# Kernel tuning notes

Hardware: AMD Instinct MI355X
Metric: run time of the kernel (lower is better)

The kernel has to match this reference:

```python
import jax, jax.numpy as jnp
import numpy as np

N_NODES = 100000
N_EDGES = 1600000
IN_FEATS = 256
N_HIDDEN = 128
N_CLASSES = 40


def setup_inputs() -> dict:
    key = jax.random.key(0)
    k1, k2, k3, k4, k5 = jax.random.split(key, 5)
    features = jax.random.normal(k1, (N_NODES, IN_FEATS), dtype=jnp.float32)
    edge_src = jax.random.randint(k2, (N_EDGES,), 0, N_NODES, dtype=jnp.int64)
    edge_dst = jax.random.randint(k3, (N_EDGES,), 0, N_NODES, dtype=jnp.int64)
    # GraphConv weights (Glorot-ish scaling)
    W1 = jax.random.normal(k4, (IN_FEATS, N_HIDDEN), dtype=jnp.float32) / np.sqrt(IN_FEATS)
    b1 = jnp.zeros((N_HIDDEN,), dtype=jnp.float32)
    W2 = jax.random.normal(k5, (N_HIDDEN, N_CLASSES), dtype=jnp.float32) / np.sqrt(N_HIDDEN)
    b2 = jnpspace = None
    b2 = jnp.zeros((N_CLASSES,), dtype=jnp.float32)
    return {"features": features, "edge_src": edge_src, "edge_dst": edge_dst,
            "W1": W1, "b1": b1, "W2": W2, "b2": b2}


def _degree_norms(edge_src, edge_dst, n_nodes):
    ones = jnp.ones(edge_src.shape[0], dtype=jnp.float32)
    deg_out = jax.ops.segment_sum(ones, edge_src, num_segments=n_nodes)
    deg_in = jax.ops.segment_sum(ones, edge_dst, num_segments=n_nodes)
    norm_src = jax.lax.rsqrt(jnp.clip(deg_out, 1.0))  # D_out^{-1/2}
    norm_dst = jax.lax.rsqrt(jnp.clip(deg_in, 1.0))   # D_in^{-1/2}
    return norm_src, norm_dst


def _graph_conv(x, W, b, edge_src, edge_dst, norm_src, norm_dst, activation=None):
    # DGL GraphConv norm='both': out = D_in^{-1/2} A D_out^{-1/2} (x W) + b
    h = (x @ W) * norm_src[:, None]                       # transform then src-normalize
    agg = jax.ops.segment_sum(h[edge_src], edge_dst,
                              num_segments=x.shape[0])    # sparse neighbor aggregation
    out = agg * norm_dst[:, None] + b
    if activation is not None:
        out = activation(out)
    return out


def reference(features, edge_src, edge_dst, W1, b1, W2, b2):
    norm_src, norm_dst = _degree_norms(edge_src, edge_dst, features.shape[0])
    h = _graph_conv(features, W1, b1, edge_src, edge_dst, norm_src, norm_dst,
                    activation=jax.nn.relu)
    # dropout is identity in eval-mode reference
    out = _graph_conv(h, W2, b2, edge_src, edge_dst, norm_src, norm_dst)
    return out
```

## Files before the change

kernel.cpp:

```cpp
#include <hip/hip_runtime.h>
#include <hip/hip_bf16.h>
#include <hip/hip_fp16.h>

#define NN 100000
#define NE 1600000
#define KF 256
#define NH 128
#define NC 40
#define CMAX 63

#define NBLK_P 512
#define PCHUNK (NE / NBLK_P)
#define BUK 256
#define NBUK ((NN + BUK - 1) / BUK)
#define CAP 6144

typedef __attribute__((ext_vector_type(8))) short bf16x8;
typedef __attribute__((ext_vector_type(4))) float f32x4;


__device__ __forceinline__ float ldf(const void* p, size_t i, bool bf){
  return bf ? __bfloat162float(((const __hip_bfloat16*)p)[i]) : ((const float*)p)[i];
}
__device__ __forceinline__ void splitbf(float f, short* h, short* lo){
  union { float f; unsigned int u; } a; a.f = f;
  *h = (short)(a.u >> 16);
  union { unsigned int u; float f; } c; c.u = a.u & 0xffff0000u;
  union { float f; unsigned int u; } d; d.f = f - c.f;
  *lo = (short)(d.u >> 16);
}

__global__ void k_sniff_edges(const unsigned int* __restrict__ e, unsigned int* __restrict__ flags){
  __shared__ unsigned int sh[256];
  unsigned int v = 0;
  for (int i = blockIdx.x * 256 + threadIdx.x; i < NE / 2; i += gridDim.x * 256)
    v |= e[2 * i + 1];
  sh[threadIdx.x] = v;
  __syncthreads();
  for (int off = 128; off; off >>= 1){
    if (threadIdx.x < off) sh[threadIdx.x] |= sh[threadIdx.x + off];
    __syncthreads();
  }
  if (threadIdx.x == 0 && sh[0]) atomicOr(&flags[0], sh[0]);
}

__global__ void k_sniff_float(const unsigned int* __restrict__ w, unsigned int* __restrict__ flags){
  __shared__ unsigned int sh[256];
  unsigned int hits = 0;
  for (int i = blockIdx.x * 256 + threadIdx.x; i < (1 << 20); i += gridDim.x * 256){
    unsigned int b = (w[i] >> 7) & 0xFFu;
    hits += (b >= 118u && b <= 130u) ? 1u : 0u;
  }
  sh[threadIdx.x] = hits;
  __syncthreads();
  for (int off = 128; off; off >>= 1){
    if (threadIdx.x < off) sh[threadIdx.x] += sh[threadIdx.x + off];
    __syncthreads();
  }
  if (threadIdx.x == 0) atomicAdd(&flags[1], sh[0]);
}

__device__ __forceinline__ int edge_at(const void* p, int e, bool is64){
  return is64 ? (int)((const long long*)p)[e] : ((const int*)p)[e];
}
__device__ __forceinline__ bool f_isbf(const unsigned int* flags){ return flags[1] > (1u << 19); }

__global__ __launch_bounds__(256) void k_part(const void* __restrict__ src,
    const void* __restrict__ dst, const unsigned int* __restrict__ flags,
    int* __restrict__ deg_out, int* __restrict__ gcur, unsigned int* __restrict__ part){
  __shared__ int cnt[NBUK];
  __shared__ int base[NBUK];
  const bool is64 = (flags[0] == 0u);
  const int beg = blockIdx.x * PCHUNK;
  const int end = min(beg + PCHUNK, NE);
  for (int t = threadIdx.x; t < NBUK; t += 256) cnt[t] = 0;
  __syncthreads();
  for (int e = beg + threadIdx.x; e < end; e += 256){
    int d = edge_at(dst, e, is64);
    atomicAdd(&cnt[d >> 8], 1);
  }
  __syncthreads();
  for (int t = threadIdx.x; t < NBUK; t += 256){
    int c = cnt[t];
    base[t] = c ? atomicAdd(&gcur[t], c) : 0;
    cnt[t] = 0;
  }
  __syncthreads();
  for (int e = beg + threadIdx.x; e < end; e += 256){
    int d = edge_at(dst, e, is64);
    int s = edge_at(src, e, is64);
    atomicAdd(&deg_out[s], 1);
    int b = d >> 8;
    int pos = base[b] + atomicAdd(&cnt[b], 1);
    if (pos < CAP)
      part[(size_t)b * CAP + pos] = ((unsigned int)s << 8) | (unsigned int)(d & 255);
  }
}

__global__ __launch_bounds__(256) void k_csr(const unsigned int* __restrict__ part,
    const int* __restrict__ gcur, int* __restrict__ fill, int* __restrict__ csr_t){
  __shared__ int rows[256 * CMAX];
  __shared__ int fl[256];
  const int b = blockIdx.x;
  fl[threadIdx.x] = 0;
  __syncthreads();
  const int n = min(gcur[b], CAP);
  for (int i = threadIdx.x; i < n; i += 256){
    unsigned int e = part[(size_t)b * CAP + i];
    int r = (int)(e & 255u);
    int s = (int)(e >> 8);
    int pos = atomicAdd(&fl[r], 1);
    if (pos < CMAX) rows[r * CMAX + pos] = s;
  }
  __syncthreads();
  const int node0 = b * BUK;
  const int node  = node0 + threadIdx.x;
  if (node < NN) fill[node] = fl[threadIdx.x];
  __syncthreads();
  for (int off = 128; off; off >>= 1){
    if (threadIdx.x < off) fl[threadIdx.x] = max(fl[threadIdx.x], fl[threadIdx.x + off]);
    __syncthreads();
  }
  const int mx = min(fl[0], CMAX);
  for (int c = 0; c < mx; c++)
    if (node < NN) csr_t[(size_t)c * NN + node] = rows[threadIdx.x * CMAX + c];
}

__global__ void k_norms(const int* __restrict__ deg_out, const int* __restrict__ fill,
                        float* __restrict__ nsrc, float* __restrict__ ndst){
  int i = blockIdx.x * 256 + threadIdx.x;
  if (i < NN){
    nsrc[i] = rsqrtf(fmaxf((float)deg_out[i], 1.f));
    ndst[i] = rsqrtf(fmaxf((float)fill[i], 1.f));
  }
}

__global__ void k_w1s_f32(const void* __restrict__ W1, const unsigned int* __restrict__ flags,
                          bf16x8* __restrict__ w1h, bf16x8* __restrict__ w1l){
  if (f_isbf(flags)) return;
  int idx = blockIdx.x * 256 + threadIdx.x;
  if (idx >= 4096) return;
  int l    = idx & 63;
  int tile = idx >> 6;
  int kt   = tile >> 3;
  int nt   = tile & 7;
  int krow = kt * 32 + (l >> 4) * 8;
  int col  = nt * 16 + (l & 15);
  const float* w = (const float*)W1;
  bf16x8 vh, vl;
  #pragma unroll
  for (int j = 0; j < 8; j++){
    short h, lo;
    splitbf(w[(size_t)(krow + j) * NH + col], &h, &lo);
    vh[j] = h; vl[j] = lo;
  }
  w1h[idx] = vh;
  w1l[idx] = vl;
}

__global__ __launch_bounds__(256) void k_gemm1_mf32(const float* __restrict__ feat,
    const bf16x8* __restrict__ w1h, const bf16x8* __restrict__ w1l,
    const unsigned int* __restrict__ flags,
    const float* __restrict__ nsrc, __half* __restrict__ h1){
  const int t  = threadIdx.x;
  const int wv = t >> 6;
  const int l  = t & 63;
  const int row0 = blockIdx.x * 128 + wv * 32;
  const int ar0 = row0 + (l & 15);
  const int ar1 = ar0 + 16;
  const float* fp0 = feat + (size_t)min(ar0, NN - 1) * KF + (l >> 4) * 8;
  const float* fp1 = feat + (size_t)min(ar1, NN - 1) * KF + (l >> 4) * 8;

  f32x4 acc[2][8];
  #pragma unroll
  for (int g = 0; g < 2; g++)
    #pragma unroll
    for (int n = 0; n < 8; n++) acc[g][n] = (f32x4){0.f, 0.f, 0.f, 0.f};

  for (int kt = 0; kt < 8; kt++){
    float4 u0 = *(const float4*)(fp0 + kt * 32);
    float4 u1 = *(const float4*)(fp0 + kt * 32 + 4);
    float4 v0 = *(const float4*)(fp1 + kt * 32);
    float4 v1 = *(const float4*)(fp1 + kt * 32 + 4);
    bf16x8 a0h, a0l, a1h, a1l;
    {
      const float* uf = (const float*)&u0;
      const float* vf = (const float*)&v0;
      #pragma unroll
      for (int j = 0; j < 4; j++){
        short h, lo;
        splitbf(uf[j], &h, &lo); a0h[j] = h; a0l[j] = lo;
        splitbf(vf[j], &h, &lo); a1h[j] = h; a1l[j] = lo;
      }
      const float* uf2 = (const float*)&u1;
      const float* vf2 = (const float*)&v1;
      #pragma unroll
      for (int j = 0; j < 4; j++){
        short h, lo;
        splitbf(uf2[j], &h, &lo); a0h[4 + j] = h; a0l[4 + j] = lo;
        splitbf(vf2[j], &h, &lo); a1h[4 + j] = h; a1l[4 + j] = lo;
      }
    }
    #pragma unroll
    for (int n = 0; n < 8; n++){
      bf16x8 bh = w1h[(kt * 8 + n) * 64 + l];
      bf16x8 bl = w1l[(kt * 8 + n) * 64 + l];
      acc[0][n] = __builtin_amdgcn_mfma_f32_16x16x32_bf16(a0h, bh, acc[0][n], 0, 0, 0);
      acc[0][n] = __builtin_amdgcn_mfma_f32_16x16x32_bf16(a0l, bh, acc[0][n], 0, 0, 0);
      acc[0][n] = __builtin_amdgcn_mfma_f32_16x16x32_bf16(a0h, bl, acc[0][n], 0, 0, 0);
      acc[1][n] = __builtin_amdgcn_mfma_f32_16x16x32_bf16(a1h, bh, acc[1][n], 0, 0, 0);
      acc[1][n] = __builtin_amdgcn_mfma_f32_16x16x32_bf16(a1l, bh, acc[1][n], 0, 0, 0);
      acc[1][n] = __builtin_amdgcn_mfma_f32_16x16x32_bf16(a1h, bl, acc[1][n], 0, 0, 0);
    }
  }
  const int col = l & 15;
  #pragma unroll
  for (int g = 0; g < 2; g++){
    const int rbase = row0 + g * 16 + (l >> 4) * 4;
    #pragma unroll
    for (int i = 0; i < 4; i++){
      int r = rbase + i;
      if (r < NN){
        float s = nsrc[r];
        #pragma unroll
        for (int n = 0; n < 8; n++)
          h1[(size_t)r * NH + n * 16 + col] = __float2half_rn(acc[g][n][i] * s);
      }
    }
  }
}

__global__ __launch_bounds__(256) void k_agg1v(const int* __restrict__ csr_t,
    const int* __restrict__ fill, const float* __restrict__ ndst,
    const __half* __restrict__ h1, const void* __restrict__ b1,
    const unsigned int* __restrict__ flags, float* __restrict__ x1){
  const bool isbf = f_isbf(flags);
  const int node = blockIdx.x * 4 + (threadIdx.x >> 6);
  if (node >= NN) return;
  const int l  = threadIdx.x & 63;
  const int g  = l >> 4;
  const int sl = l & 15;
  const int deg = min(fill[node], CMAX);
  float a[8] = {0.f,0.f,0.f,0.f,0.f,0.f,0.f,0.f};
  int c0 = 0;
  for (; c0 + 8 <= deg; c0 += 8){
    int s0 = csr_t[(size_t)(c0 + g) * NN + node];
    int s1 = csr_t[(size_t)(c0 + 4 + g) * NN + node];
    uint4 u0 = *(const uint4*)(h1 + (size_t)s0 * NH + sl * 8);
    uint4 u1 = *(const uint4*)(h1 + (size_t)s1 * NH + sl * 8);
    const __half2* h0 = (const __half2*)&u0;
    const __half2* hp1 = (const __half2*)&u1;
    #pragma unroll
    for (int j = 0; j < 4; j++){
      float2 v0 = __half22float2(h0[j]);
      float2 v1 = __half22float2(hp1[j]);
      a[2*j]   += v0.x + v1.x;
      a[2*j+1] += v0.y + v1.y;
    }
  }
  for (; c0 < deg; c0 += 4){
    int c = c0 + g;
    if (c < deg){
      int s = csr_t[(size_t)c * NN + node];
      uint4 u = *(const uint4*)(h1 + (size_t)s * NH + sl * 8);
      const __half2* hp = (const __half2*)&u;
      #pragma unroll
      for (int j = 0; j < 4; j++){
        float2 v = __half22float2(hp[j]);
        a[2*j]   += v.x;
        a[2*j+1] += v.y;
      }
    }
  }
  #pragma unroll
  for (int j = 0; j < 8; j++){
    a[j] += __shfl_xor(a[j], 16);
    a[j] += __shfl_xor(a[j], 32);
  }
  if (g == 0){
    float nd = ndst[node];
    float o[8];
    #pragma unroll
    for (int j = 0; j < 8; j++)
      o[j] = fmaxf(a[j] * nd + ldf(b1, sl * 8 + j, isbf), 0.f);
    float4* xp = (float4*)(x1 + (size_t)node * NH + sl * 8);
    xp[0] = make_float4(o[0], o[1], o[2], o[3]);
    xp[1] = make_float4(o[4], o[5], o[6], o[7]);
  }
}

__global__ __launch_bounds__(256) void k_gemm2(const float* __restrict__ x1,
    const void* __restrict__ W2, const unsigned int* __restrict__ flags,
    const float* __restrict__ nsrc, __half* __restrict__ h2){
  const bool isbf = f_isbf(flags);
  __shared__ float Xs[128][68];
  __shared__ float Ws[64][44];
  const int t = threadIdx.x;
  const int row0 = blockIdx.x * 128;
  const int cg = t & 7;
  const int rg = t >> 3;
  float acc[4][5];
  #pragma unroll
  for (int i = 0; i < 4; i++)
    #pragma unroll
    for (int j = 0; j < 5; j++) acc[i][j] = 0.f;

  for (int kc = 0; kc < NH; kc += 64){
    #pragma unroll
    for (int q0 = 0; q0 < 8; q0++){
      int q  = t + q0 * 256;
      int r  = q >> 4;
      int kq = (q & 15) * 4;
      int grow = row0 + r;
      float4 v;
      if (grow < NN) v = *(const float4*)(x1 + (size_t)grow * NH + kc + kq);
      else { v.x = v.y = v.z = v.w = 0.f; }
      *(float4*)&Xs[r][kq] = v;
    }
    #pragma unroll
    for (int q0 = 0; q0 < 10; q0++){
      int idx = t + q0 * 256;
      int k = idx / 40;
      int c = idx - k * 40;
      Ws[k][c] = ldf(W2, (size_t)(kc + k) * NC + c, isbf);
    }
    __syncthreads();
    #pragma unroll 4
    for (int k = 0; k < 64; k++){
      float a0 = Xs[rg*4+0][k];
      float a1 = Xs[rg*4+1][k];
      float a2 = Xs[rg*4+2][k];
      float a3 = Xs[rg*4+3][k];
      float b[5];
      #pragma unroll
      for (int j = 0; j < 5; j++) b[j] = Ws[k][cg*5 + j];
      #pragma unroll
      for (int j = 0; j < 5; j++){
        acc[0][j] += a0 * b[j];
        acc[1][j] += a1 * b[j];
        acc[2][j] += a2 * b[j];
        acc[3][j] += a3 * b[j];
      }
    }
    __syncthreads();
  }
  #pragma unroll
  for (int i = 0; i < 4; i++){
    int r = row0 + rg*4 + i;
    if (r < NN){
      float s = nsrc[r];
      #pragma unroll
      for (int j = 0; j < 5; j++)
        h2[(size_t)r * NC + cg*5 + j] = __float2half_rn(acc[i][j] * s);
    }
  }
}

__global__ __launch_bounds__(256) void k_agg2v(const int* __restrict__ csr_t,
    const int* __restrict__ fill, const float* __restrict__ ndst,
    const __half* __restrict__ h2, const void* __restrict__ b2,
    const unsigned int* __restrict__ flags, float* __restrict__ out){
  const bool isbf = f_isbf(flags);
  const int node = blockIdx.x * 4 + (threadIdx.x >> 6);
  if (node >= NN) return;
  const int l  = threadIdx.x & 63;
  const int g  = l >> 4;
  const int sl = l & 15;
  const int deg = min(fill[node], CMAX);
  float a[4] = {0.f,0.f,0.f,0.f};
  if (sl < 10){
    int c0 = 0;
    for (; c0 + 8 <= deg; c0 += 8){
      int s0 = csr_t[(size_t)(c0 + g) * NN + node];
      int s1 = csr_t[(size_t)(c0 + 4 + g) * NN + node];
      uint2 u0 = *(const uint2*)(h2 + (size_t)s0 * NC + sl * 4);
      uint2 u1 = *(const uint2*)(h2 + (size_t)s1 * NC + sl * 4);
      const __half2* h0 = (const __half2*)&u0;
      const __half2* hp1 = (const __half2*)&u1;
      #pragma unroll
      for (int j = 0; j < 2; j++){
        float2 v0 = __half22float2(h0[j]);
        float2 v1 = __half22float2(hp1[j]);
        a[2*j]   += v0.x + v1.x;
        a[2*j+1] += v0.y + v1.y;
      }
    }
    for (; c0 < deg; c0 += 4){
      int c = c0 + g;
      if (c < deg){
        int s = csr_t[(size_t)c * NN + node];
        uint2 u = *(const uint2*)(h2 + (size_t)s * NC + sl * 4);
        const __half2* hp = (const __half2*)&u;
        #pragma unroll
        for (int j = 0; j < 2; j++){
          float2 v = __half22float2(hp[j]);
          a[2*j]   += v.x;
          a[2*j+1] += v.y;
        }
      }
    }
  }
  #pragma unroll
  for (int j = 0; j < 4; j++){
    a[j] += __shfl_xor(a[j], 16);
    a[j] += __shfl_xor(a[j], 32);
  }
  if (g == 0 && sl < 10){
    float nd = ndst[node];
    float4 o;
    o.x = a[0] * nd + ldf(b2, sl * 4 + 0, isbf);
    o.y = a[1] * nd + ldf(b2, sl * 4 + 1, isbf);
    o.z = a[2] * nd + ldf(b2, sl * 4 + 2, isbf);
    o.w = a[3] * nd + ldf(b2, sl * 4 + 3, isbf);
    *(float4*)(out + (size_t)node * NC + sl * 4) = o;
  }
}

extern "C" void kernel_launch(void* const* d_in, const int* in_sizes, int n_in,
                              void* d_out, int out_size, void* d_ws, size_t ws_size,
                              hipStream_t stream) {
  const long long SZ_FEAT = (long long)NN * KF, SZ_E = NE, SZ_W1 = (long long)KF * NH,
                  SZ_B1 = NH, SZ_W2 = (long long)NH * NC, SZ_B2 = NC;
  int i_feat = -1, i_e1 = -1, i_e2 = -1, i_W1 = -1, i_b1 = -1, i_W2 = -1, i_b2 = -1;
  auto m = [](long long s, long long z){ return s == z || s == 4*z || s == 8*z || s == 2*z; };
  for (int i = 0; i < n_in; i++){
    long long s = in_sizes[i];
    if      (m(s, SZ_FEAT)) i_feat = i;
    else if (m(s, SZ_E))    { if (i_e1 < 0) i_e1 = i; else i_e2 = i; }
    else if (m(s, SZ_W1))   i_W1 = i;
    else if (m(s, SZ_B1))   i_b1 = i;
    else if (m(s, SZ_W2))   i_W2 = i;
    else if (m(s, SZ_B2))   i_b2 = i;
  }
  if (i_feat < 0 || i_e2 < 0 || i_W1 < 0 || i_b1 < 0 || i_W2 < 0 || i_b2 < 0){
    i_feat = 0; i_e1 = 1; i_e2 = 2; i_W1 = 3; i_b1 = 4; i_W2 = 5; i_b2 = 6;
  }
  const void* feat = d_in[i_feat];
  const void* esrc = d_in[i_e1];
  const void* edst = d_in[i_e2];
  const void* W1   = d_in[i_W1];
  const void* b1   = d_in[i_b1];
  const void* W2   = d_in[i_W2];
  const void* b2   = d_in[i_b2];
  float* out = (float*)d_out;

  int* deg_out        = (int*)d_ws;
  int* fill           = deg_out + NN;
  unsigned int* flags = (unsigned int*)(fill + NN);
  int* gcur           = (int*)(flags + 4);
  float* norm_src     = (float*)(gcur + 400);
  float* norm_dst     = norm_src + NN;
  int* csr_t          = (int*)(norm_dst + NN);
  __half* h1          = (__half*)(csr_t + (size_t)CMAX * NN);
  float* x1           = (float*)(h1 + (size_t)NN * NH);
  __half* h2          = h1;
  unsigned int* part  = (unsigned int*)x1;
  bf16x8* w1h         = (bf16x8*)((char*)x1 + (16u << 20));
  bf16x8* w1l         = w1h + 4096;

  hipMemsetAsync(deg_out, 0, ((size_t)2 * NN + 4 + 400) * sizeof(int), stream);

  k_sniff_edges<<<400, 256, 0, stream>>>((const unsigned int*)esrc, flags);
  k_sniff_float<<<256, 256, 0, stream>>>((const unsigned int*)feat, flags);
  k_w1s_f32<<<16, 256, 0, stream>>>(W1, flags, w1h, w1l);
  k_part<<<NBLK_P, 256, 0, stream>>>(esrc, edst, flags, deg_out, gcur, part);
  k_csr <<<NBUK,   256, 0, stream>>>(part, gcur, fill, csr_t);
  k_norms<<<(NN + 255) / 256, 256, 0, stream>>>(deg_out, fill, norm_src, norm_dst);

  k_gemm1_mf32<<<(NN + 127) / 128, 256, 0, stream>>>((const float*)feat, w1h, w1l,
                                                     flags, norm_src, h1);
  k_agg1v<<<(NN + 3) / 4, 256, 0, stream>>>(csr_t, fill, norm_dst, h1, b1, flags, x1);
  k_gemm2<<<(NN + 127) / 128, 256, 0, stream>>>(x1, W2, flags, norm_src, h2);
  k_agg2v<<<(NN + 3) / 4, 256, 0, stream>>>(csr_t, fill, norm_dst, h2, b2, flags, out);
}
```

Before: 509.4 us.

## Use feature-chunked column layout for h1/x1 and chunk-parallel layer-1 aggregation

Stores h1 and x1 as 8 column blocks of 16 features. Layer-1 aggregation then runs one feature chunk per block, with 16 edges per node processed in parallel, so each gather pass touches a much smaller working set that may stay in cache. gemm1 and gemm2 indexing are adapted to the new layout, and nontemporal loads and stores are used for the index and output streams. In exchange, CSR indices and degrees are reread once per chunk, and each gather is a smaller 16-byte access.

After: 662.7 us. +30.1%, slower.

```diff
diff --git a/kernel.cpp b/kernel.cpp
--- a/kernel.cpp
+++ b/kernel.cpp
@@ -224,45 +224,32 @@
         float s = nsrc[r];
         #pragma unroll
         for (int n = 0; n < 8; n++)
-          h1[(size_t)r * NH + n * 16 + col] = __float2half_rn(acc[g][n][i] * s);
-      }
-    }
-  }
-}
-
-__global__ __launch_bounds__(256) void k_agg1v(const int* __restrict__ csr_t,
+          h1[((size_t)n * NN + r) * 16 + col] = __float2half_rn(acc[g][n][i] * s);
+      }
+    }
+  }
+}
+
+__global__ __launch_bounds__(256) void k_agg1cw(const int* __restrict__ csr_t,
     const int* __restrict__ fill, const float* __restrict__ ndst,
-    const __half* __restrict__ h1, const void* __restrict__ b1,
-    const unsigned int* __restrict__ flags, float* __restrict__ x1){
+    const __half* __restrict__ h1c, const void* __restrict__ b1,
+    const unsigned int* __restrict__ flags, float* __restrict__ x1c){
   const bool isbf = f_isbf(flags);
-  const int node = blockIdx.x * 4 + (threadIdx.x >> 6);
-  if (node >= NN) return;
-  const int l  = threadIdx.x & 63;
-  const int g  = l >> 4;
-  const int sl = l & 15;
-  const int deg = min(fill[node], CMAX);
+  const int g    = blockIdx.x & 7;
+  const int wv   = threadIdx.x >> 6;
+  const int l    = threadIdx.x & 63;
+  const int nsub = l >> 5;
+  const int node = (blockIdx.x >> 3) * 8 + wv * 2 + nsub;
+  const int es   = (l >> 1) & 15;
+  const int half = l & 1;
+  const __half* hb = h1c + (size_t)g * NN * 16;
+  const int deg = min(__builtin_nontemporal_load(&fill[node]), CMAX);
   float a[8] = {0.f,0.f,0.f,0.f,0.f,0.f,0.f,0.f};
-  int c0 = 0;
-  for (; c0 + 8 <= deg; c0 += 8){
-    int s0 = csr_t[(size_t)(c0 + g) * NN + node];
-    int s1 = csr_t[(size_t)(c0 + 4 + g) * NN + node];
-    uint4 u0 = *(const uint4*)(h1 + (size_t)s0 * NH + sl * 8);
-    uint4 u1 = *(const uint4*)(h1 + (size_t)s1 * NH + sl * 8);
-    const __half2* h0 = (const __half2*)&u0;
-    const __half2* hp1 = (const __half2*)&u1;
-    #pragma unroll
-    for (int j = 0; j < 4; j++){
-      float2 v0 = __half22float2(h0[j]);
-      float2 v1 = __half22float2(hp1[j]);
-      a[2*j]   += v0.x + v1.x;
-      a[2*j+1] += v0.y + v1.y;
-    }
-  }
-  for (; c0 < deg; c0 += 4){
-    int c = c0 + g;
+  for (int c0 = 0; c0 < deg; c0 += 16){
+    int c = c0 + es;
     if (c < deg){
-      int s = csr_t[(size_t)c * NN + node];
-      uint4 u = *(const uint4*)(h1 + (size_t)s * NH + sl * 8);
+      int s = __builtin_nontemporal_load(&csr_t[(size_t)c * NN + node]);
+      uint4 u = *(const uint4*)(hb + (size_t)s * 16 + half * 8);
       const __half2* hp = (const __half2*)&u;
       #pragma unroll
       for (int j = 0; j < 4; j++){
@@ -274,22 +261,27 @@
   }
   #pragma unroll
   for (int j = 0; j < 8; j++){
+    a[j] += __shfl_xor(a[j], 2);
+    a[j] += __shfl_xor(a[j], 4);
+    a[j] += __shfl_xor(a[j], 8);
     a[j] += __shfl_xor(a[j], 16);
-    a[j] += __shfl_xor(a[j], 32);
-  }
-  if (g == 0){
+  }
+  if (es == 0){
     float nd = ndst[node];
-    float o[8];
-    #pragma unroll
-    for (int j = 0; j < 8; j++)
-      o[j] = fmaxf(a[j] * nd + ldf(b1, sl * 8 + j, isbf), 0.f);
-    float4* xp = (float4*)(x1 + (size_t)node * NH + sl * 8);
-    xp[0] = make_float4(o[0], o[1], o[2], o[3]);
-    xp[1] = make_float4(o[4], o[5], o[6], o[7]);
-  }
-}
-
-__global__ __launch_bounds__(256) void k_gemm2(const float* __restrict__ x1,
+    int f0 = g * 16 + half * 8;
+    f32x4 o0, o1;
+    #pragma unroll
+    for (int j = 0; j < 4; j++){
+      o0[j] = fmaxf(a[j]     * nd + ldf(b1, f0 + j,     isbf), 0.f);
+      o1[j] = fmaxf(a[4 + j] * nd + ldf(b1, f0 + 4 + j, isbf), 0.f);
+    }
+    f32x4* xp = (f32x4*)(x1c + ((size_t)g * NN + node) * 16 + half * 8);
+    __builtin_nontemporal_store(o0, xp);
+    __builtin_nontemporal_store(o1, xp + 1);
+  }
+}
+
+__global__ __launch_bounds__(256) void k_gemm2(const float* __restrict__ x1c,
     const void* __restrict__ W2, const unsigned int* __restrict__ flags,
     const float* __restrict__ nsrc, __half* __restrict__ h2){
   const bool isbf = f_isbf(flags);
@@ -312,8 +304,10 @@
       int r  = q >> 4;
       int kq = (q & 15) * 4;
       int grow = row0 + r;
+      int colc = kc + kq;
       float4 v;
-      if (grow < NN) v = *(const float4*)(x1 + (size_t)grow * NH + kc + kq);
+      if (grow < NN)
+        v = *(const float4*)(x1c + ((size_t)(colc >> 4) * NN + grow) * 16 + (colc & 15));
       else { v.x = v.y = v.z = v.w = 0.f; }
       *(float4*)&Xs[r][kq] = v;
     }
@@ -469,7 +463,7 @@
 
   k_gemm1_mf32<<<(NN + 127) / 128, 256, 0, stream>>>((const float*)feat, w1h, w1l,
                                                      flags, norm_src, h1);
-  k_agg1v<<<(NN + 3) / 4, 256, 0, stream>>>(csr_t, fill, norm_dst, h1, b1, flags, x1);
+  k_agg1cw<<<(NN / 8) * 8, 256, 0, stream>>>(csr_t, fill, norm_dst, h1, b1, flags, x1);
   k_gemm2<<<(NN + 127) / 128, 256, 0, stream>>>(x1, W2, flags, norm_src, h2);
   k_agg2v<<<(NN + 3) / 4, 256, 0, stream>>>(csr_t, fill, norm_dst, h2, b2, flags, out);
 }
```
